# Kernel optimization log

Measured on AMD Instinct MI355X. Metric: run time of the kernel, lower is better.

Reference implementation:

```python
import jax, jax.numpy as jnp
import numpy as np

N_NODES = 100000
IN_CH = 128
HID_CH = 128
N_EDGES = 1600000


def setup_inputs() -> dict:
    key = jax.random.key(0)
    ks = jax.random.split(key, 8)
    x = jax.random.normal(ks[0], (N_NODES, IN_CH), dtype=jnp.float32)
    edge_index = jax.random.randint(ks[1], (2, N_EDGES), 0, N_NODES, dtype=jnp.int64)
    s1 = 1.0 / np.sqrt(IN_CH)
    s2 = 1.0 / np.sqrt(HID_CH)
    # SAGEConv layer 1: lin_l (aggregated neighbors, has bias), lin_r (root)
    Wl1 = jax.random.uniform(ks[2], (IN_CH, HID_CH), jnp.float32, -s1, s1)
    Wr1 = jax.random.uniform(ks[3], (IN_CH, HID_CH), jnp.float32, -s1, s1)
    b1 = jnp.zeros((HID_CH,), jnp.float32)
    # SAGEConv layer 2
    Wl2 = jax.random.uniform(ks[4], (HID_CH, HID_CH), jnp.float32, -s2, s2)
    Wr2 = jax.random.uniform(ks[5], (HID_CH, HID_CH), jnp.float32, -s2, s2)
    b2 = jnp.zeros((HID_CH,), jnp.float32)
    return {"x": x, "edge_index": edge_index,
            "Wl1": Wl1, "Wr1": Wr1, "b1": b1,
            "Wl2": Wl2, "Wr2": Wr2, "b2": b2}


def _sage_conv(x, src, dst, inv_deg, Wl, Wr, b):
    # mean aggregation of source-node features into destination nodes
    agg = jax.ops.segment_sum(x[src], dst, num_segments=N_NODES)  # [N, d]
    mean = agg * inv_deg[:, None]
    # out = lin_l(mean_neighbors) + lin_r(x)
    return mean @ Wl + x @ Wr + b


def reference(x, edge_index, Wl1, Wr1, b1, Wl2, Wr2, b2):
    src = edge_index[0]
    dst = edge_index[1]
    deg = jax.ops.segment_sum(jnp.ones_like(dst, dtype=jnp.float32), dst,
                              num_segments=N_NODES)
    inv_deg = 1.0 / jnp.maximum(deg, 1.0)
    h = jax.nn.relu(_sage_conv(x, src, dst, inv_deg, Wl1, Wr1, b1))
    # F.dropout(p=0.2, training=False) is identity in eval mode
    h = jax.nn.relu(_sage_conv(h, src, dst, inv_deg, Wl2, Wr2, b2))
    return h
```

## Files before the change

### kernel.cpp

```cpp
#include <hip/hip_runtime.h>

#define NN 100000
#define NE 1600000
#define CH 128

#define PART 512
#define NP 196
#define PCAP 8704
#define EPB 4096
#define NB 391
#define SCAP 64
#define SLAB 1536

typedef __attribute__((ext_vector_type(8))) short bf16x8;
typedef __attribute__((ext_vector_type(4))) float f32x4;
typedef __attribute__((ext_vector_type(4))) unsigned int u32x4;
typedef unsigned int uint;
typedef unsigned short ushort;

__device__ __forceinline__ ushort f2b(float f) {
    uint u = __builtin_bit_cast(uint, f);
    uint r = (u + 0x7fff + ((u >> 16) & 1)) >> 16;
    return (ushort)r;
}
__device__ __forceinline__ float blo(uint v) { return __builtin_bit_cast(float, v << 16); }
__device__ __forceinline__ float bhi(uint v) { return __builtin_bit_cast(float, v & 0xffff0000u); }

__device__ __forceinline__ void acc8(float* a, uint4 v) {
    a[0] += blo(v.x); a[1] += bhi(v.x);
    a[2] += blo(v.y); a[3] += bhi(v.y);
    a[4] += blo(v.z); a[5] += bhi(v.z);
    a[6] += blo(v.w); a[7] += bhi(v.w);
}


__global__ __launch_bounds__(1024) void k_bin(const int4* __restrict__ src4, const int4* __restrict__ dst4,
                                              uint* __restrict__ pcnt, uint* __restrict__ pairbuf) {
    __shared__ uint slots[NP * SCAP];
    __shared__ uint lcnt[NP];
    __shared__ uint lbase[NP];
    int tid = threadIdx.x;
    if (tid < NP) lcnt[tid] = 0;
    __syncthreads();
    int e4 = blockIdx.x * 1024 + tid;
    if (e4 < NE / 4) {
        int4 d4 = dst4[e4];
        int4 s4 = src4[e4];
        int dd[4] = {d4.x, d4.y, d4.z, d4.w};
        int ss[4] = {s4.x, s4.y, s4.z, s4.w};
        #pragma unroll
        for (int j = 0; j < 4; ++j) {
            int p = dd[j] >> 9;
            uint pair = ((uint)(dd[j] & 511) << 17) | (uint)ss[j];
            uint pos = atomicAdd(&lcnt[p], 1u);
            if (pos < SCAP) slots[p * SCAP + pos] = pair;
        }
    }
    __syncthreads();
    if (tid < NP) {
        uint c = lcnt[tid];
        c = c < SCAP ? c : SCAP;
        lcnt[tid] = c;
        lbase[tid] = atomicAdd(&pcnt[tid], c);
    }
    __syncthreads();
    for (int t = tid; t < NP * SCAP; t += 1024) {
        int p = t >> 6;
        uint s = (uint)(t & (SCAP - 1));
        if (s < lcnt[p]) {
            uint idx = lbase[p] + s;
            if (idx < PCAP) pairbuf[(size_t)p * PCAP + idx] = slots[t];
        }
    }
}


__global__ __launch_bounds__(512) void k_csr(const uint* __restrict__ pcnt, const uint* __restrict__ pairbuf,
                                             int* __restrict__ nbrG, uint* __restrict__ pack) {
    __shared__ uint pairs[PCAP];
    __shared__ uint cnt[PART];
    __shared__ uint rowptr[PART + 1];
    __shared__ uint wpart[8];
    int tid = threadIdx.x;
    int p = blockIdx.x;
    uint tot = pcnt[p];
    tot = tot < PCAP ? tot : PCAP;
    for (uint i = tid; i < tot; i += 512) pairs[i] = pairbuf[(size_t)p * PCAP + i];
    cnt[tid] = 0;
    __syncthreads();
    for (uint i = tid; i < tot; i += 512) atomicAdd(&cnt[pairs[i] >> 17], 1u);
    __syncthreads();
    uint deg = cnt[tid];
    uint s = deg;
    #pragma unroll
    for (int off = 1; off < 64; off <<= 1) {
        uint t = __shfl_up(s, off, 64);
        if ((tid & 63) >= off) s += t;
    }
    if ((tid & 63) == 63) wpart[tid >> 6] = s;
    __syncthreads();
    uint base = 0;
    int w = tid >> 6;
    #pragma unroll
    for (int q = 0; q < 7; ++q) base += (q < w) ? wpart[q] : 0;
    rowptr[tid] = base + s - deg;
    if (tid == 511) rowptr[512] = base + s;
    cnt[tid] = 0;
    __syncthreads();
    for (uint i = tid; i < tot; i += 512) {
        uint u = pairs[i];
        uint dl = u >> 17;
        uint pos = rowptr[dl] + atomicAdd(&cnt[dl], 1u);
        nbrG[(size_t)p * PCAP + pos] = (int)(u & 0x1FFFFu);
    }
    {
        int n = p * PART + tid;
        if (n < NN) {
            uint d = rowptr[tid + 1] - rowptr[tid];
            pack[n] = ((uint)(p * PCAP) + rowptr[tid]) | (d << 21);
        }
    }
}


__global__ __launch_bounds__(256) void k_castx(const float* __restrict__ x, ushort* __restrict__ xb,
                                               const float* __restrict__ Wl1, const float* __restrict__ Wr1,
                                               const float* __restrict__ Wl2, const float* __restrict__ Wr2,
                                               ushort* __restrict__ BtK1, ushort* __restrict__ BtK2) {
    int p = blockIdx.y;
    if (p == 4) {
        int i = blockIdx.x * 256 + threadIdx.x;
        if (i >= 65536) return;
        int L = i >> 15;
        int ii = i & 32767;
        const float* Wl = L ? Wl2 : Wl1;
        const float* Wr = L ? Wr2 : Wr1;
        ushort* BtK = L ? BtK2 : BtK1;
        int c = ii & 31;
        int n = (ii >> 5) & 127;
        int kt = ii >> 12;
        int k = kt * 32 + c;
        float v = (k < 128) ? Wl[k * 128 + n] : Wr[(k - 128) * 128 + n];
        BtK[ii] = f2b(v);
        return;
    }
    int n = blockIdx.x * 256 + threadIdx.x;
    if (n >= NN) return;
    const float4* sp = (const float4*)(x + (size_t)n * 128 + p * 32);
    uint4 o[4];
    ushort* op = (ushort*)o;
    #pragma unroll
    for (int q = 0; q < 8; ++q) {
        float4 v = sp[q];
        op[q * 4 + 0] = f2b(v.x);
        op[q * 4 + 1] = f2b(v.y);
        op[q * 4 + 2] = f2b(v.z);
        op[q * 4 + 3] = f2b(v.w);
    }
    uint4* dp = (uint4*)(xb + ((size_t)p * NN + n) * 32);
    #pragma unroll
    for (int q = 0; q < 4; ++q) dp[q] = o[q];
}


__global__ __launch_bounds__(256) void k_agg(const uint4* __restrict__ feat, const int* __restrict__ nbrG,
                                             const uint* __restrict__ pack, uint* __restrict__ outb) {
    __shared__ int sl[SLAB];
    __shared__ int sh_s0, sh_cnt;
    int plane = blockIdx.x;
    int nb = blockIdx.y * 64;
    int tid = threadIdx.x;
    int n = nb + (tid >> 2);
    int h = tid & 3;
    if (tid == 0) {
        uint u0 = pack[nb];
        int last = nb + 63 < NN ? nb + 63 : NN - 1;
        uint u1 = pack[last];
        int s0 = (int)(u0 & 0x1FFFFFu);
        sh_s0 = s0;
        sh_cnt = (int)(u1 & 0x1FFFFFu) + (int)(u1 >> 21) - s0;
    }
    __syncthreads();
    int s0 = sh_s0, scnt = sh_cnt;
    bool staged = scnt <= SLAB;
    if (staged) {
        for (int i = tid; i < scnt; i += 256) sl[i] = __builtin_nontemporal_load(&nbrG[s0 + i]);
    }
    __syncthreads();
    if (n >= NN) return;
    uint u = pack[n];
    int s = (int)(u & 0x1FFFFFu);
    int d = (int)(u >> 21);
    const char* fb = (const char*)feat + ((size_t)plane * NN) * 64;
    uint hoff = (uint)h * 16;
    float a[8] = {};
    if (staged) {
        const int* bp = sl + (s - s0);
        int i = 0;
        for (; i + 8 <= d; i += 8) {
            uint off[8];
            uint4 v[8];
            #pragma unroll
            for (int j = 0; j < 8; ++j) off[j] = ((uint)bp[i + j] << 6) | hoff;
            #pragma unroll
            for (int j = 0; j < 8; ++j) v[j] = *(const uint4*)(fb + off[j]);
            #pragma unroll
            for (int j = 0; j < 8; ++j) acc8(a, v[j]);
        }
        for (; i < d; ++i) acc8(a, *(const uint4*)(fb + (((uint)bp[i] << 6) | hoff)));
    } else {
        const int* bp = nbrG + s;
        int i = 0;
        for (; i + 4 <= d; i += 4) {
            uint o0 = ((uint)bp[i] << 6) | hoff;
            uint o1 = ((uint)bp[i + 1] << 6) | hoff;
            uint o2 = ((uint)bp[i + 2] << 6) | hoff;
            uint o3 = ((uint)bp[i + 3] << 6) | hoff;
            uint4 v0 = *(const uint4*)(fb + o0);
            uint4 v1 = *(const uint4*)(fb + o1);
            uint4 v2 = *(const uint4*)(fb + o2);
            uint4 v3 = *(const uint4*)(fb + o3);
            acc8(a, v0);
            acc8(a, v1);
            acc8(a, v2);
            acc8(a, v3);
        }
        for (; i < d; ++i) acc8(a, *(const uint4*)(fb + (((uint)bp[i] << 6) | hoff)));
    }
    float id = 1.0f / fmaxf((float)d, 1.0f);
    u32x4 r;
    r.x = (uint)f2b(a[0] * id) | ((uint)f2b(a[1] * id) << 16);
    r.y = (uint)f2b(a[2] * id) | ((uint)f2b(a[3] * id) << 16);
    r.z = (uint)f2b(a[4] * id) | ((uint)f2b(a[5] * id) << 16);
    r.w = (uint)f2b(a[6] * id) | ((uint)f2b(a[7] * id) << 16);
    __builtin_nontemporal_store(r, (u32x4*)(outb + (((size_t)plane * NN + n) * 4 + h) * 4));
}


template <bool WB16>
__global__ __launch_bounds__(256) void k_gemm(const ushort* __restrict__ Am, const ushort* Ax,
                                              const ushort* __restrict__ BtK, const float* __restrict__ bias,
                                              void* outp, int M) {
    int lane = threadIdx.x & 63;
    int wave = threadIdx.x >> 6;
    int bm = blockIdx.x * 128 + wave * 32;
    int l16 = lane & 15;
    int lk8 = (lane >> 4) * 8;

    f32x4 acc[2][8] = {};
    #pragma unroll
    for (int kt = 0; kt < 8; ++kt) {
        const ushort* A = (kt < 4) ? Am : Ax;
        int p = kt & 3;
        bf16x8 af[2];
        #pragma unroll
        for (int mt = 0; mt < 2; ++mt) {
            int row = bm + mt * 16 + l16;
            row = row < M ? row : M - 1;
            af[mt] = *(const bf16x8*)(A + ((size_t)p * NN + row) * 32 + lk8);
        }
        const ushort* Bk = BtK + (size_t)kt * 128 * 32;
        #pragma unroll
        for (int nt = 0; nt < 8; ++nt) {
            bf16x8 bfr = *(const bf16x8*)(Bk + (size_t)(nt * 16 + l16) * 32 + lk8);
            acc[0][nt] = __builtin_amdgcn_mfma_f32_16x16x32_bf16(af[0], bfr, acc[0][nt], 0, 0, 0);
            acc[1][nt] = __builtin_amdgcn_mfma_f32_16x16x32_bf16(af[1], bfr, acc[1][nt], 0, 0, 0);
        }
    }
    int mr0 = (lane >> 4) * 4;
    #pragma unroll
    for (int mt = 0; mt < 2; ++mt) {
        #pragma unroll
        for (int r = 0; r < 4; ++r) {
            int m = bm + mt * 16 + mr0 + r;
            if (m < M) {
                #pragma unroll
                for (int nt = 0; nt < 8; ++nt) {
                    float v = acc[mt][nt][r] + bias[nt * 16 + l16];
                    v = v > 0.f ? v : 0.f;
                    if (WB16) {
                        int ch = nt * 16 + l16;
                        ((ushort*)outp)[((size_t)(ch >> 5) * NN + m) * 32 + (ch & 31)] = f2b(v);
                    } else {
                        ((float*)outp)[(size_t)m * 128 + nt * 16 + l16] = v;
                    }
                }
            }
        }
    }
}


static inline size_t alignup(size_t x) { return (x + 255) & ~(size_t)255; }

extern "C" void kernel_launch(void* const* d_in, const int* in_sizes, int n_in,
                              void* d_out, int out_size, void* d_ws, size_t ws_size,
                              hipStream_t stream) {
    const float* x   = (const float*)d_in[0];
    const int* edge  = (const int*)d_in[1];
    const float* Wl1 = (const float*)d_in[2];
    const float* Wr1 = (const float*)d_in[3];
    const float* b1  = (const float*)d_in[4];
    const float* Wl2 = (const float*)d_in[5];
    const float* Wr2 = (const float*)d_in[6];
    const float* b2  = (const float*)d_in[7];
    float* out = (float*)d_out;

    const int* srcp = edge;
    const int* dstp = edge + NE;

    uint* pairbuf = (uint*)d_out;
    int* nbrG = (int*)d_out + (size_t)NP * PCAP;

    char* w = (char*)d_ws;
    uint* pcnt = (uint*)w;     w += alignup((size_t)NP * 4);
    uint* pack = (uint*)w;     w += alignup((size_t)NN * 4);
    ushort* xb = (ushort*)w;   w += alignup((size_t)NN * CH * 2);
    ushort* mb = (ushort*)w;   w += alignup((size_t)NN * CH * 2);
    ushort* BtK1 = (ushort*)w; w += alignup((size_t)128 * 256 * 2);
    ushort* BtK2 = (ushort*)w; w += alignup((size_t)128 * 256 * 2);

    hipMemsetAsync(pcnt, 0, (size_t)NP * 4, stream);

    k_bin<<<NB, 1024, 0, stream>>>((const int4*)srcp, (const int4*)dstp, pcnt, pairbuf);
    k_csr<<<NP, 512, 0, stream>>>(pcnt, pairbuf, nbrG, pack);

    k_castx<<<dim3((NN + 255) / 256, 5), 256, 0, stream>>>(x, xb, Wl1, Wr1, Wl2, Wr2, BtK1, BtK2);

    int gg = (NN + 127) / 128;
    dim3 ag(4, (NN + 63) / 64);
    k_agg<<<ag, 256, 0, stream>>>((const uint4*)xb, nbrG, pack, (uint*)mb);
    k_gemm<true><<<gg, 256, 0, stream>>>(mb, xb, BtK1, b1, (void*)xb, NN);
    k_agg<<<ag, 256, 0, stream>>>((const uint4*)xb, nbrG, pack, (uint*)mb);
    k_gemm<false><<<gg, 256, 0, stream>>>(mb, xb, BtK2, b2, (void*)out, NN);
}
```

Baseline: 347.5 us.

## Sort CSR neighbor lists by source bucket and drop nontemporal hints in aggregation

The CSR build now counts edges per destination in 8 sub-buckets keyed on the source index's high bits, then places neighbors so each row is roughly ordered by source region. Gathers in the aggregation kernel then touch feature memory in more localized address ranges, aiming for better L2/MALL reuse. Separately, the nontemporal load of neighbor indices and the nontemporal store of the aggregated output become ordinary accesses, so the output can stay in cache for the following GEMM. The cost is an 8x larger shared counter array and extra prefix work in the CSR kernel.

```diff
diff --git a/kernel.cpp b/kernel.cpp
--- a/kernel.cpp
+++ b/kernel.cpp
@@ -14,7 +14,6 @@
 
 typedef __attribute__((ext_vector_type(8))) short bf16x8;
 typedef __attribute__((ext_vector_type(4))) float f32x4;
-typedef __attribute__((ext_vector_type(4))) unsigned int u32x4;
 typedef unsigned int uint;
 typedef unsigned short ushort;
 
@@ -78,7 +77,7 @@
 __global__ __launch_bounds__(512) void k_csr(const uint* __restrict__ pcnt, const uint* __restrict__ pairbuf,
                                              int* __restrict__ nbrG, uint* __restrict__ pack) {
     __shared__ uint pairs[PCAP];
-    __shared__ uint cnt[PART];
+    __shared__ uint cnt8[PART * 8];
     __shared__ uint rowptr[PART + 1];
     __shared__ uint wpart[8];
     int tid = threadIdx.x;
@@ -86,11 +85,22 @@
     uint tot = pcnt[p];
     tot = tot < PCAP ? tot : PCAP;
     for (uint i = tid; i < tot; i += 512) pairs[i] = pairbuf[(size_t)p * PCAP + i];
-    cnt[tid] = 0;
-    __syncthreads();
-    for (uint i = tid; i < tot; i += 512) atomicAdd(&cnt[pairs[i] >> 17], 1u);
-    __syncthreads();
-    uint deg = cnt[tid];
+    #pragma unroll
+    for (int b = 0; b < 8; ++b) cnt8[tid * 8 + b] = 0;
+    __syncthreads();
+    for (uint i = tid; i < tot; i += 512) {
+        uint u = pairs[i];
+        atomicAdd(&cnt8[(u >> 17) * 8 + ((u & 0x1FFFFu) >> 14)], 1u);
+    }
+    __syncthreads();
+    uint run = 0;
+    #pragma unroll
+    for (int b = 0; b < 8; ++b) {
+        uint t = cnt8[tid * 8 + b];
+        cnt8[tid * 8 + b] = run;
+        run += t;
+    }
+    uint deg = run;
     uint s = deg;
     #pragma unroll
     for (int off = 1; off < 64; off <<= 1) {
@@ -105,13 +115,13 @@
     for (int q = 0; q < 7; ++q) base += (q < w) ? wpart[q] : 0;
     rowptr[tid] = base + s - deg;
     if (tid == 511) rowptr[512] = base + s;
-    cnt[tid] = 0;
     __syncthreads();
     for (uint i = tid; i < tot; i += 512) {
         uint u = pairs[i];
         uint dl = u >> 17;
-        uint pos = rowptr[dl] + atomicAdd(&cnt[dl], 1u);
-        nbrG[(size_t)p * PCAP + pos] = (int)(u & 0x1FFFFu);
+        uint src = u & 0x1FFFFu;
+        uint pos = rowptr[dl] + atomicAdd(&cnt8[dl * 8 + (src >> 14)], 1u);
+        nbrG[(size_t)p * PCAP + pos] = (int)src;
     }
     {
         int n = p * PART + tid;
@@ -164,7 +174,7 @@
 
 
 __global__ __launch_bounds__(256) void k_agg(const uint4* __restrict__ feat, const int* __restrict__ nbrG,
-                                             const uint* __restrict__ pack, uint* __restrict__ outb) {
+                                             const uint* __restrict__ pack, uint4* __restrict__ outb) {
     __shared__ int sl[SLAB];
     __shared__ int sh_s0, sh_cnt;
     int plane = blockIdx.x;
@@ -184,7 +194,7 @@
     int s0 = sh_s0, scnt = sh_cnt;
     bool staged = scnt <= SLAB;
     if (staged) {
-        for (int i = tid; i < scnt; i += 256) sl[i] = __builtin_nontemporal_load(&nbrG[s0 + i]);
+        for (int i = tid; i < scnt; i += 256) sl[i] = nbrG[s0 + i];
     }
     __syncthreads();
     if (n >= NN) return;
@@ -228,12 +238,12 @@
         for (; i < d; ++i) acc8(a, *(const uint4*)(fb + (((uint)bp[i] << 6) | hoff)));
     }
     float id = 1.0f / fmaxf((float)d, 1.0f);
-    u32x4 r;
+    uint4 r;
     r.x = (uint)f2b(a[0] * id) | ((uint)f2b(a[1] * id) << 16);
     r.y = (uint)f2b(a[2] * id) | ((uint)f2b(a[3] * id) << 16);
     r.z = (uint)f2b(a[4] * id) | ((uint)f2b(a[5] * id) << 16);
     r.w = (uint)f2b(a[6] * id) | ((uint)f2b(a[7] * id) << 16);
-    __builtin_nontemporal_store(r, (u32x4*)(outb + (((size_t)plane * NN + n) * 4 + h) * 4));
+    outb[((size_t)plane * NN + n) * 4 + h] = r;
 }
 
 
@@ -329,8 +339,8 @@
 
     int gg = (NN + 127) / 128;
     dim3 ag(4, (NN + 63) / 64);
-    k_agg<<<ag, 256, 0, stream>>>((const uint4*)xb, nbrG, pack, (uint*)mb);
+    k_agg<<<ag, 256, 0, stream>>>((const uint4*)xb, nbrG, pack, (uint4*)mb);
     k_gemm<true><<<gg, 256, 0, stream>>>(mb, xb, BtK1, b1, (void*)xb, NN);
-    k_agg<<<ag, 256, 0, stream>>>((const uint4*)xb, nbrG, pack, (uint*)mb);
+    k_agg<<<ag, 256, 0, stream>>>((const uint4*)xb, nbrG, pack, (uint4*)mb);
     k_gemm<false><<<gg, 256, 0, stream>>>(mb, xb, BtK2, b2, (void*)out, NN);
 }
```

Result: faster. 334.2 us (-3.8%).

## Fuse x/weight bf16 cast into edge binning kernel; drop nontemporal hints in aggregation

Applied to the files above, without the earlier changes.

Merges the x-to-bf16 and weight-packing cast kernel into the edge binning kernel as extra blocks, so the casts run alongside binning and one launch disappears. The cast blocks now use 1024 threads but still allocate the large static shared arrays of the binning path, which may limit how many of them run at once. The aggregation kernel also switches its neighbor-list loads and output stores from nontemporal builtins to ordinary loads and stores, changing how they are cached.

```diff
diff --git a/kernel.cpp b/kernel.cpp
--- a/kernel.cpp
+++ b/kernel.cpp
@@ -7,14 +7,12 @@
 #define PART 512
 #define NP 196
 #define PCAP 8704
-#define EPB 4096
 #define NB 391
 #define SCAP 64
 #define SLAB 1536
 
 typedef __attribute__((ext_vector_type(8))) short bf16x8;
 typedef __attribute__((ext_vector_type(4))) float f32x4;
-typedef __attribute__((ext_vector_type(4))) unsigned int u32x4;
 typedef unsigned int uint;
 typedef unsigned short ushort;
 
@@ -34,15 +32,56 @@
 }
 
 
-__global__ __launch_bounds__(1024) void k_bin(const int4* __restrict__ src4, const int4* __restrict__ dst4,
-                                              uint* __restrict__ pcnt, uint* __restrict__ pairbuf) {
+__global__ __launch_bounds__(1024) void k_pre(const int4* __restrict__ src4, const int4* __restrict__ dst4,
+                                              uint* __restrict__ pcnt, uint* __restrict__ pairbuf,
+                                              const float* __restrict__ x, ushort* __restrict__ xb,
+                                              const float* __restrict__ Wl1, const float* __restrict__ Wr1,
+                                              const float* __restrict__ Wl2, const float* __restrict__ Wr2,
+                                              ushort* __restrict__ BtK1, ushort* __restrict__ BtK2) {
     __shared__ uint slots[NP * SCAP];
     __shared__ uint lcnt[NP];
     __shared__ uint lbase[NP];
     int tid = threadIdx.x;
+    int b = blockIdx.x;
+    if (b >= NB) {
+        int i = b - NB;
+        if (i < 392) {
+            int p = i / 98;
+            int n = (i % 98) * 1024 + tid;
+            if (n >= NN) return;
+            const float4* sp = (const float4*)(x + (size_t)n * 128 + p * 32);
+            uint4 o[4];
+            ushort* op = (ushort*)o;
+            #pragma unroll
+            for (int q = 0; q < 8; ++q) {
+                float4 v = sp[q];
+                op[q * 4 + 0] = f2b(v.x);
+                op[q * 4 + 1] = f2b(v.y);
+                op[q * 4 + 2] = f2b(v.z);
+                op[q * 4 + 3] = f2b(v.w);
+            }
+            uint4* dp = (uint4*)(xb + ((size_t)p * NN + n) * 32);
+            #pragma unroll
+            for (int q = 0; q < 4; ++q) dp[q] = o[q];
+        } else {
+            int idx = (i - 392) * 1024 + tid;
+            int L = idx >> 15;
+            int ii = idx & 32767;
+            const float* Wl = L ? Wl2 : Wl1;
+            const float* Wr = L ? Wr2 : Wr1;
+            ushort* BtK = L ? BtK2 : BtK1;
+            int c = ii & 31;
+            int n = (ii >> 5) & 127;
+            int kt = ii >> 12;
+            int k = kt * 32 + c;
+            float v = (k < 128) ? Wl[k * 128 + n] : Wr[(k - 128) * 128 + n];
+            BtK[ii] = f2b(v);
+        }
+        return;
+    }
     if (tid < NP) lcnt[tid] = 0;
     __syncthreads();
-    int e4 = blockIdx.x * 1024 + tid;
+    int e4 = b * 1024 + tid;
     if (e4 < NE / 4) {
         int4 d4 = dst4[e4];
         int4 s4 = src4[e4];
@@ -123,48 +162,8 @@
 }
 
 
-__global__ __launch_bounds__(256) void k_castx(const float* __restrict__ x, ushort* __restrict__ xb,
-                                               const float* __restrict__ Wl1, const float* __restrict__ Wr1,
-                                               const float* __restrict__ Wl2, const float* __restrict__ Wr2,
-                                               ushort* __restrict__ BtK1, ushort* __restrict__ BtK2) {
-    int p = blockIdx.y;
-    if (p == 4) {
-        int i = blockIdx.x * 256 + threadIdx.x;
-        if (i >= 65536) return;
-        int L = i >> 15;
-        int ii = i & 32767;
-        const float* Wl = L ? Wl2 : Wl1;
-        const float* Wr = L ? Wr2 : Wr1;
-        ushort* BtK = L ? BtK2 : BtK1;
-        int c = ii & 31;
-        int n = (ii >> 5) & 127;
-        int kt = ii >> 12;
-        int k = kt * 32 + c;
-        float v = (k < 128) ? Wl[k * 128 + n] : Wr[(k - 128) * 128 + n];
-        BtK[ii] = f2b(v);
-        return;
-    }
-    int n = blockIdx.x * 256 + threadIdx.x;
-    if (n >= NN) return;
-    const float4* sp = (const float4*)(x + (size_t)n * 128 + p * 32);
-    uint4 o[4];
-    ushort* op = (ushort*)o;
-    #pragma unroll
-    for (int q = 0; q < 8; ++q) {
-        float4 v = sp[q];
-        op[q * 4 + 0] = f2b(v.x);
-        op[q * 4 + 1] = f2b(v.y);
-        op[q * 4 + 2] = f2b(v.z);
-        op[q * 4 + 3] = f2b(v.w);
-    }
-    uint4* dp = (uint4*)(xb + ((size_t)p * NN + n) * 32);
-    #pragma unroll
-    for (int q = 0; q < 4; ++q) dp[q] = o[q];
-}
-
-
 __global__ __launch_bounds__(256) void k_agg(const uint4* __restrict__ feat, const int* __restrict__ nbrG,
-                                             const uint* __restrict__ pack, uint* __restrict__ outb) {
+                                             const uint* __restrict__ pack, uint4* __restrict__ outb) {
     __shared__ int sl[SLAB];
     __shared__ int sh_s0, sh_cnt;
     int plane = blockIdx.x;
@@ -184,7 +183,7 @@
     int s0 = sh_s0, scnt = sh_cnt;
     bool staged = scnt <= SLAB;
     if (staged) {
-        for (int i = tid; i < scnt; i += 256) sl[i] = __builtin_nontemporal_load(&nbrG[s0 + i]);
+        for (int i = tid; i < scnt; i += 256) sl[i] = nbrG[s0 + i];
     }
     __syncthreads();
     if (n >= NN) return;
@@ -228,12 +227,12 @@
         for (; i < d; ++i) acc8(a, *(const uint4*)(fb + (((uint)bp[i] << 6) | hoff)));
     }
     float id = 1.0f / fmaxf((float)d, 1.0f);
-    u32x4 r;
+    uint4 r;
     r.x = (uint)f2b(a[0] * id) | ((uint)f2b(a[1] * id) << 16);
     r.y = (uint)f2b(a[2] * id) | ((uint)f2b(a[3] * id) << 16);
     r.z = (uint)f2b(a[4] * id) | ((uint)f2b(a[5] * id) << 16);
     r.w = (uint)f2b(a[6] * id) | ((uint)f2b(a[7] * id) << 16);
-    __builtin_nontemporal_store(r, (u32x4*)(outb + (((size_t)plane * NN + n) * 4 + h) * 4));
+    outb[((size_t)plane * NN + n) * 4 + h] = r;
 }
 
 
@@ -322,15 +321,14 @@
 
     hipMemsetAsync(pcnt, 0, (size_t)NP * 4, stream);
 
-    k_bin<<<NB, 1024, 0, stream>>>((const int4*)srcp, (const int4*)dstp, pcnt, pairbuf);
+    k_pre<<<NB + 392 + 64, 1024, 0, stream>>>((const int4*)srcp, (const int4*)dstp, pcnt, pairbuf,
+                                              x, xb, Wl1, Wr1, Wl2, Wr2, BtK1, BtK2);
     k_csr<<<NP, 512, 0, stream>>>(pcnt, pairbuf, nbrG, pack);
-
-    k_castx<<<dim3((NN + 255) / 256, 5), 256, 0, stream>>>(x, xb, Wl1, Wr1, Wl2, Wr2, BtK1, BtK2);
 
     int gg = (NN + 127) / 128;
     dim3 ag(4, (NN + 63) / 64);
-    k_agg<<<ag, 256, 0, stream>>>((const uint4*)xb, nbrG, pack, (uint*)mb);
+    k_agg<<<ag, 256, 0, stream>>>((const uint4*)xb, nbrG, pack, (uint4*)mb);
     k_gemm<true><<<gg, 256, 0, stream>>>(mb, xb, BtK1, b1, (void*)xb, NN);
-    k_agg<<<ag, 256, 0, stream>>>((const uint4*)xb, nbrG, pack, (uint*)mb);
+    k_agg<<<ag, 256, 0, stream>>>((const uint4*)xb, nbrG, pack, (uint4*)mb);
     k_gemm<false><<<gg, 256, 0, stream>>>(mb, xb, BtK2, b2, (void*)out, NN);
 }
```

Measured after the change: 339.3 us. -2.4%, faster.
